# Kernel optimization log

Hardware: AMD Instinct MI355X
Metric: run time of the kernel (lower is better)

The kernel has to match this reference:

```python
import jax, jax.numpy as jnp
import numpy as np

B = 32
SEQ_LEN = 512      # T and n_fft
PRED_LEN = 96      # STFT window_size = PRED_LEN // 2 = 48
TOP_K = 3
D_MODEL = 512
D_FF = 512
N_HEADS = 8
C_OUT = 32         # graph node count
NODE_DIM = 10
CONV_CH = 32
SKIP_CH = 32
GCN_DEPTH = 2
PROP_ALPHA = 0.05
HOP = 48
EPS = 1e-5


def layer_norm(x, g, b):
    m = x.mean(-1, keepdims=True)
    v = ((x - m) ** 2).mean(-1, keepdims=True)
    return (x - m) * jax.lax.rsqrt(v + EPS) * g + b


def stft_mag(x):
    """torch.stft(center=True, hann window of len 48 center-padded to n_fft) magnitude,
    vmapped over channels. Returns [B, frames, n_fft//2+1, N]."""
    n_fft = SEQ_LEN
    win_len = PRED_LEN // 2
    n = jnp.arange(win_len, dtype=x.dtype)
    win = 0.5 - 0.5 * jnp.cos(2.0 * jnp.pi * n / win_len)   # periodic hann
    pad_l = (n_fft - win_len) // 2
    win = jnp.pad(win, (pad_l, n_fft - win_len - pad_l))     # center-pad window to n_fft
    T = x.shape[1]
    xp = jnp.pad(x, ((0, 0), (n_fft // 2, n_fft // 2), (0, 0)), mode='reflect')
    nfr = T // HOP + 1
    idx = jnp.arange(nfr)[:, None] * HOP + jnp.arange(n_fft)[None, :]
    frames = xp[:, idx, :]                                   # [B, nfr, n_fft, N]
    spec = jnp.fft.rfft(frames * win[None, None, :, None], axis=2)
    return jnp.abs(spec)


def attention_block(x, wq, bq, wk, bk, wv, bv, wo, bo, ff1_w, ff1_b, ff2_w, ff2_b,
                    n1_g, n1_b, n2_g, n2_b):
    M, S, D = x.shape
    H, Dh = N_HEADS, D // N_HEADS
    q = (x @ wq.T + bq).reshape(M, S, H, Dh)
    k = (x @ wk.T + bk).reshape(M, S, H, Dh)
    v = (x @ wv.T + bv).reshape(M, S, H, Dh)
    scores = jnp.einsum('mshd,mthd->mhst', q, k) * (1.0 / float(np.sqrt(Dh)))
    o = jnp.einsum('mhst,mthd->mshd', jax.nn.softmax(scores, axis=-1), v).reshape(M, S, D)
    x1 = layer_norm(x + (o @ wo.T + bo), n1_g, n1_b)
    y = jax.nn.gelu(x1 @ ff1_w.T + ff1_b, approximate=False) @ ff2_w.T + ff2_b
    return layer_norm(x1 + y, n2_g, n2_b)


def graph_block(x, nv1, nv2, sw, sb, mw, mb, ew, eb, lw, lb, g, b):
    # adaptive adjacency over C_OUT nodes
    adp = jax.nn.softmax(jax.nn.relu(nv1 @ nv2), axis=1)
    adj = adp + jnp.eye(C_OUT, dtype=x.dtype)
    a = adj / adj.sum(1, keepdims=True)
    # start_conv: [B,1,D,T] -> [B,CONV_CH,C_OUT,T]
    h = jax.lax.conv_general_dilated(x.transpose(0, 2, 1)[:, None], sw, (1, 1), 'VALID',
                                     dimension_numbers=('NCHW', 'OIHW', 'NCHW'))
    h = h + sb[None, :, None, None]
    x0, outs = h, [h]
    for _ in range(GCN_DEPTH):  # mixprop
        h = PROP_ALPHA * x0 + (1.0 - PROP_ALPHA) * jnp.einsum('bcwt,vw->bcvt', h, a)
        outs.append(h)
    ho = jnp.einsum('oc,bcnt->bont', mw, jnp.concatenate(outs, axis=1)) + mb[None, :, None, None]
    h = jax.nn.gelu(ho, approximate=False)
    out = jnp.einsum('bcns,tcs->btn', h, ew) + eb[None, :, None]   # end_conv (1,seq_len) kernel
    out = out @ lw + lb                                            # Linear c_out -> d_model
    return layer_norm(x + out, g, b)


def setup_inputs() -> dict:
    ks = jax.random.split(jax.random.key(0), 32)
    r = lambda i, shape, s=0.02: jax.random.normal(ks[i], shape, jnp.float32) * s
    kh = D_MODEL - C_OUT + 1
    return {
        'x': jax.random.normal(ks[0], (B, SEQ_LEN, D_MODEL), jnp.float32),
        'nv1': r(1, (TOP_K, C_OUT, NODE_DIM), 1.0),
        'nv2': r(2, (TOP_K, NODE_DIM, C_OUT), 1.0),
        'start_w': r(3, (TOP_K, CONV_CH, 1, kh, 1)),
        'start_b': r(4, (TOP_K, CONV_CH)),
        'mix_w': r(5, (TOP_K, SKIP_CH, (GCN_DEPTH + 1) * CONV_CH)),
        'mix_b': r(6, (TOP_K, SKIP_CH)),
        'end_w': r(7, (TOP_K, SEQ_LEN, SKIP_CH, SEQ_LEN)),
        'end_b': r(8, (TOP_K, SEQ_LEN)),
        'glin_w': r(9, (TOP_K, C_OUT, D_MODEL)),
        'glin_b': r(10, (TOP_K, D_MODEL)),
        'gnorm_g': 1.0 + r(11, (TOP_K, D_MODEL), 0.1),
        'gnorm_b': r(12, (TOP_K, D_MODEL), 0.1),
        'wq': r(13, (D_MODEL, D_MODEL)), 'bq': r(14, (D_MODEL,)),
        'wk': r(15, (D_MODEL, D_MODEL)), 'bk': r(16, (D_MODEL,)),
        'wv': r(17, (D_MODEL, D_MODEL)), 'bv': r(18, (D_MODEL,)),
        'wo': r(19, (D_MODEL, D_MODEL)), 'bo': r(20, (D_MODEL,)),
        'ff1_w': r(21, (D_FF, D_MODEL)), 'ff1_b': r(22, (D_FF,)),
        'ff2_w': r(23, (D_MODEL, D_FF)), 'ff2_b': r(24, (D_MODEL,)),
        'an1_g': 1.0 + r(25, (D_MODEL,), 0.1), 'an1_b': r(26, (D_MODEL,), 0.1),
        'an2_g': 1.0 + r(27, (D_MODEL,), 0.1), 'an2_b': r(28, (D_MODEL,), 0.1),
        'norm_g': 1.0 + r(29, (D_MODEL,), 0.1), 'norm_b': r(30, (D_MODEL,), 0.1),
    }


def reference(x, nv1, nv2, start_w, start_b, mix_w, mix_b, end_w, end_b, glin_w, glin_b,
              gnorm_g, gnorm_b, wq, bq, wk, bk, wv, bv, wo, bo,
              ff1_w, ff1_b, ff2_w, ff2_b, an1_g, an1_b, an2_g, an2_b, norm_g, norm_b):
    Bx, T, N = x.shape
    mag = stft_mag(x)                                   # [B, frames, Fbins, N]
    freq = mag.mean(axis=(0, 1, 3)).at[0].set(0.0)
    top = np.asarray(jax.lax.top_k(freq, TOP_K)[1])     # concrete: shapes below are data-dependent
    periods = [int(T // int(f)) for f in top]
    sw = jax.nn.softmax(mag[:, :, top, :].mean(axis=(1, 3)), axis=1)  # [B, k] scale weights
    cur = x
    res = []
    for i in range(TOP_K):
        scale = periods[i]
        # NOTE: faithful to the original bug: x is overwritten by gconv output each iteration
        cur = graph_block(cur, nv1[i], nv2[i], start_w[i], start_b[i], mix_w[i], mix_b[i],
                          end_w[i], end_b[i], glin_w[i], glin_b[i], gnorm_g[i], gnorm_b[i])
        length = -(-T // scale) * scale
        out = jnp.pad(cur, ((0, 0), (0, length - T), (0, 0))) if length > T else cur
        out = out.reshape(Bx * (length // scale), scale, N)
        out = attention_block(out, wq, bq, wk, bk, wv, bv, wo, bo,
                              ff1_w, ff1_b, ff2_w, ff2_b, an1_g, an1_b, an2_g, an2_b)
        out = jax.nn.gelu(layer_norm(out, norm_g, norm_b), approximate=False)
        out = out.reshape(Bx, length, N)[:, :T]
        res.append(out)
    res = jnp.stack(res, axis=-1)                       # [B, T, N, k]
    return (res * sw[:, None, None, :]).sum(-1) + cur
```

## Files before the change

### kernel.cpp

```cpp
#include <hip/hip_runtime.h>
#include <math.h>

#define DI __device__ __forceinline__

namespace {
constexpr int B_ = 32;
constexpr int T_ = 512;
constexpr int N_ = 512;
constexpr int C_ = 32;
constexpr int KH_ = 481;
constexpr int HOP_ = 48;
constexpr int WIN_ = 48;
constexpr int NFR_ = 11;
constexpr int NBIN_ = 257;
constexpr int NSB_ = 8 * NFR_ * B_;
constexpr int TOKMAX = 21760;
constexpr int PLW = TOKMAX * 512;
constexpr float EPS_ = 1e-5f;

constexpr size_t MBY = 1ull << 20;
constexpr size_t OFF_META = 0;
constexpr size_t OFF_FREQ = 4096;
constexpr size_t OFF_SW   = 8192;
constexpr size_t OFF_BEFF = 16384;
constexpr size_t OFF_P12  = 32768;
constexpr size_t OFF_FSB  = 65536;
constexpr size_t OFF_OSM  = 1 * MBY;
constexpr size_t OFF_WB   = 4 * MBY;
constexpr size_t OFF_WDH  = 10 * MBY;
constexpr size_t OFF_EWH  = 12 * MBY;
constexpr size_t OFF_CUR  = 44 * MBY;
constexpr size_t OFF_ACC  = 76 * MBY;
constexpr size_t TR       = 108 * MBY;
constexpr size_t OFF_T    = TR;
constexpr size_t OFF_WPH  = TR + 6 * MBY;
constexpr size_t OFF_G    = TR + 64 * MBY;
constexpr size_t OFF_G2   = TR + 128 * MBY;
constexpr size_t OFF_PART = TR + 192 * MBY;
constexpr size_t OFF_A0 = TR;
constexpr size_t OFF_A2 = TR + 44 * MBY;
constexpr size_t OFF_A3 = TR + 88 * MBY;
constexpr size_t OFF_A4 = TR + 132 * MBY;
constexpr size_t OFF_A5 = TR + 176 * MBY;
constexpr size_t OFF_FP = TR;
}

typedef __attribute__((ext_vector_type(2))) float f32x2;
typedef __attribute__((ext_vector_type(4))) float f32x4;
typedef __attribute__((ext_vector_type(8))) short bf8;
typedef __attribute__((ext_vector_type(8))) unsigned short u16x8;

DI float gelu_exact(float x) { return 0.5f * x * (1.0f + erff(x * 0.7071067811865475f)); }
DI unsigned short f2bf(float f) {
  unsigned u = __float_as_uint(f);
  u += 0x7FFFu + ((u >> 16) & 1u);
  return (unsigned short)(u >> 16);
}
DI float bf2f(unsigned short s) { return __uint_as_float(((unsigned)s) << 16); }
DI float ld2(const unsigned short* __restrict__ H, const unsigned short* __restrict__ L,
             size_t i) { return bf2f(H[i]) + bf2f(L[i]); }
DI void st2(unsigned short* __restrict__ H, unsigned short* __restrict__ L,
            size_t i, float v) {
  unsigned short h = f2bf(v);
  H[i] = h;
  L[i] = f2bf(v - bf2f(h));
}
DI void gll16(const unsigned short* g, unsigned short* l) {
  __builtin_amdgcn_global_load_lds(
      (const __attribute__((address_space(1))) void*)g,
      (__attribute__((address_space(3))) void*)l, 16, 0, 0);
}

__global__ __launch_bounds__(256) void k_stft2(const float* __restrict__ x,
                                               float* __restrict__ fpart) {
  int bid = blockIdx.x;
  int cc = bid & 7;
  int f = (bid >> 3) % NFR_;
  int b = bid / (8 * NFR_);
  __shared__ float xw[WIN_][64];
  int tid = threadIdx.x;
  for (int i = tid; i < WIN_ * 64; i += 256) {
    int j = i >> 6, n = i & 63;
    int gi = f * HOP_ + 232 + j - 256;
    if (gi < 0) gi = -gi;
    float w = 0.5f - 0.5f * cosf((float)j * 0.13089969389957472f);
    xw[j][n] = w * x[((size_t)b * T_ + gi) * N_ + cc * 64 + n];
  }
  __syncthreads();
  for (int pair = tid; pair < NBIN_ * 8; pair += 256) {
    int k = pair >> 3;
    int c4 = (pair & 7) * 4;
    int r0 = (k * 232) & 511;
    float a0 = (float)r0 * 0.012271846303085130f;
    float c = cosf(a0), s = sinf(a0);
    float dA = (float)k * 0.012271846303085130f;
    float cd = cosf(dA), sd = sinf(dA);
    f32x2 ri[8];
#pragma unroll
    for (int q = 0; q < 8; ++q) ri[q] = (f32x2){0.f, 0.f};
#pragma unroll 4
    for (int j = 0; j < WIN_; ++j) {
      float4 v0 = *(const float4*)&xw[j][c4];
      float4 v1 = *(const float4*)&xw[j][32 + c4];
      f32x2 cs = (f32x2){c, s};
      ri[0] += v0.x * cs;
      ri[1] += v0.y * cs;
      ri[2] += v0.z * cs;
      ri[3] += v0.w * cs;
      ri[4] += v1.x * cs;
      ri[5] += v1.y * cs;
      ri[6] += v1.z * cs;
      ri[7] += v1.w * cs;
      float cn = c * cd - s * sd;
      s = s * cd + c * sd;
      c = cn;
    }
    float m = 0.f;
#pragma unroll
    for (int q = 0; q < 8; ++q) m += sqrtf(ri[q].x * ri[q].x + ri[q].y * ri[q].y);
    for (int off = 4; off > 0; off >>= 1) m += __shfl_xor(m, off);
    if ((tid & 7) == 0) fpart[(size_t)k * NSB_ + bid] = m;
  }
}

__global__ __launch_bounds__(256) void k_fred(const float* __restrict__ fpart,
                                              float* __restrict__ freq,
                                              float* __restrict__ fsumb) {
  int k = blockIdx.x;
  int tid = threadIdx.x;
  int b = tid >> 3, j = tid & 7;
  float s = 0.f;
  for (int i = j; i < 88; i += 8) s += fpart[(size_t)k * NSB_ + b * 88 + i];
  for (int off = 4; off > 0; off >>= 1) s += __shfl_xor(s, off);
  __shared__ float bs[32];
  if (j == 0) bs[b] = s;
  __syncthreads();
  if (tid < 32) {
    float v = bs[tid];
    fsumb[k * 32 + tid] = v;
    for (int off = 16; off > 0; off >>= 1) v += __shfl_xor(v, off);
    if (tid == 0) freq[k] = v;
  }
}

__global__ void k_topk(const float* __restrict__ freq, const float* __restrict__ fsumb,
                       int* __restrict__ meta, float* __restrict__ swb) {
  __shared__ int stop[3];
  int tid = threadIdx.x;
  if (tid == 0) {
    float bv[3] = {-1e30f, -1e30f, -1e30f};
    int bi[3] = {1, 1, 1};
    for (int k = 1; k < NBIN_; ++k) {
      float v = freq[k];
      if (v > bv[0]) { bv[2]=bv[1]; bi[2]=bi[1]; bv[1]=bv[0]; bi[1]=bi[0]; bv[0]=v; bi[0]=k; }
      else if (v > bv[1]) { bv[2]=bv[1]; bi[2]=bi[1]; bv[1]=v; bi[1]=k; }
      else if (v > bv[2]) { bv[2]=v; bi[2]=k; }
    }
    for (int i = 0; i < 3; ++i) {
      int top = bi[i];
      int p = T_ / top;
      int L = ((T_ + p - 1) / p) * p;
      meta[i] = top;
      meta[3 + i] = p;
      meta[6 + i] = L;
      meta[9 + i] = L / p;
      meta[15 + i] = B_ * L;
      stop[i] = top;
    }
  }
  __syncthreads();
  int b = tid;
  if (b < B_) {
    float inv = 1.0f / (float)(NFR_ * N_);
    float m0 = fsumb[stop[0] * 32 + b] * inv;
    float m1 = fsumb[stop[1] * 32 + b] * inv;
    float m2 = fsumb[stop[2] * 32 + b] * inv;
    float mx = fmaxf(m0, fmaxf(m1, m2));
    float e0 = expf(m0 - mx), e1 = expf(m1 - mx), e2 = expf(m2 - mx);
    float s = e0 + e1 + e2;
    swb[b * 4 + 0] = e0 / s; swb[b * 4 + 1] = e1 / s; swb[b * 4 + 2] = e2 / s;
  }
}

__global__ __launch_bounds__(1024) void k_adjprep(const float* __restrict__ nv1,
                                                  const float* __restrict__ nv2,
                                                  const float* __restrict__ mw,
                                                  const float* __restrict__ mb,
                                                  const float* __restrict__ sb,
                                                  float* __restrict__ P12,
                                                  float* __restrict__ beff) {
  __shared__ float A32s[32][32];
  __shared__ float Ms[32][32], P1s[32][32], P2s[32][32], S1[32], S2[32], sbl[32];
  int tid = threadIdx.x;
  if (tid < 32) {
    int v = tid;
    float row[32];
    for (int w = 0; w < 32; ++w) {
      float s = 0.f;
      for (int d = 0; d < 10; ++d) s += nv1[v * 10 + d] * nv2[d * 32 + w];
      row[w] = fmaxf(s, 0.f);
    }
    float mx = -1e30f;
    for (int w = 0; w < 32; ++w) mx = fmaxf(mx, row[w]);
    float sm = 0.f;
    for (int w = 0; w < 32; ++w) { row[w] = expf(row[w] - mx); sm += row[w]; }
    for (int w = 0; w < 32; ++w) row[w] /= sm;
    row[v] += 1.0f;
    float rs = 0.f;
    for (int w = 0; w < 32; ++w) rs += row[w];
    for (int w = 0; w < 32; ++w) A32s[v][w] = row[w] / rs;
    sbl[tid] = sb[tid];
  }
  __syncthreads();
  int w = tid >> 5, v = tid & 31;
  Ms[w][v] = A32s[v][w];
  __syncthreads();
  float p1 = 0.95f * Ms[w][v] + (w == v ? 0.05f : 0.f);
  P1s[w][v] = p1;
  __syncthreads();
  float p2 = 0.f;
  for (int u = 0; u < 32; ++u) p2 += P1s[w][u] * Ms[u][v];
  p2 = 0.95f * p2 + (w == v ? 0.05f : 0.f);
  P2s[w][v] = p2;
  P12[tid] = p1;
  P12[1024 + tid] = p2;
  __syncthreads();
  if (tid < 32) {
    float s1 = 0.f, s2 = 0.f;
    for (int u = 0; u < 32; ++u) { s1 += P1s[u][tid]; s2 += P2s[u][tid]; }
    S1[tid] = s1; S2[tid] = s2;
  }
  __syncthreads();
  int o = w;
  float be = mb[o];
  for (int c = 0; c < 32; ++c) {
    float sc = sbl[c];
    be += mw[o * 96 + c] * sc;
    be += mw[o * 96 + 32 + c] * sc * S1[v];
    be += mw[o * 96 + 64 + c] * sc * S2[v];
  }
  beff[tid] = be;
}

__global__ __launch_bounds__(256) void k_T(const float* __restrict__ P12,
                                           const float* __restrict__ mw,
                                           float* __restrict__ Tm) {
  int idx = blockIdx.x * 256 + threadIdx.x;
  int r = idx >> 10, k2 = idx & 1023;
  int o = r >> 5, v = r & 31;
  int c = k2 >> 5, w = k2 & 31;
  float t = mw[o * 96 + 32 + c] * P12[w * 32 + v]
          + mw[o * 96 + 64 + c] * P12[1024 + w * 32 + v];
  if (w == v) t += mw[o * 96 + c];
  Tm[idx] = t;
}

__global__ void k_wdh(const float* __restrict__ swi, unsigned short* __restrict__ WH) {
  int idx = blockIdx.x * 256 + threadIdx.x;
  int j = idx >> 10, k2 = idx & 1023;
  int c = k2 >> 5, w = k2 & 31;
  int kk = j - w;
  float vv = (kk >= 0 && kk < KH_) ? swi[c * KH_ + kk] : 0.f;
  WH[idx] = f2bf(vv);
}

__global__ void k_splith(const float* __restrict__ src, unsigned short* __restrict__ Hi,
                         int n) {
  int i = blockIdx.x * 256 + threadIdx.x;
  if (i * 4 >= n) return;
  float4 v = *(const float4*)&src[i * 4];
  ushort4 h;
  h.x = f2bf(v.x); h.y = f2bf(v.y); h.z = f2bf(v.z); h.w = f2bf(v.w);
  *(ushort4*)&Hi[i * 4] = h;
}

__global__ __launch_bounds__(256, 2) void k_mm2(
    const float* __restrict__ A, const unsigned short* __restrict__ Bh,
    const float* __restrict__ bias,
    float* __restrict__ C, float* __restrict__ Cpart,
    int M, int N, int K, int lda, int dogelu) {
  const int bm = blockIdx.y * 128;
  if (bm >= M) return;
  const int bn = blockIdx.x * 128;
  const int nz = gridDim.z, z = blockIdx.z;
  const int kpb = K / nz;
  const int kbeg = z * kpb, kend = kbeg + kpb;

  __shared__ __align__(16) unsigned short AhS[4096], AlS[4096], BhS[4096];

  const int tid = threadIdx.x;
  const int wave = tid >> 6, lane = tid & 63;
  const int wr = wave >> 1, wc = wave & 1;
  const int fr = lane & 15, fs = lane >> 4;

  const int sr = tid >> 1, ss = (tid & 1) * 2;
  const int sx = (sr >> 1) & 3;
  const int so0 = sr * 32 + 8 * (ss ^ sx);
  const int so1 = sr * 32 + 8 * ((ss + 1) ^ sx);

  const int row0 = tid >> 2;
  const int s0 = (tid & 3) ^ ((row0 >> 1) & 3);
  const unsigned short* gBh0 = Bh + (size_t)(bn + row0) * K + s0 * 8;
  const unsigned short* gBh1 = gBh0 + (size_t)64 * K;
  unsigned short* lB0 = &BhS[wave * 512];
  unsigned short* lB1 = &BhS[2048 + wave * 512];

  int aoff[4], boff[4];
#pragma unroll
  for (int m = 0; m < 4; ++m) {
    int ra = wr * 64 + m * 16 + fr;
    aoff[m] = ra * 32 + 8 * (fs ^ ((ra >> 1) & 3));
    int rb = wc * 64 + m * 16 + fr;
    boff[m] = rb * 32 + 8 * (fs ^ ((rb >> 1) & 3));
  }

  const bool aok = (bm + sr) < M;
  const float* Arow = A + (size_t)(bm + sr) * lda + ss * 8;

  f32x4 acc[4][4];
#pragma unroll
  for (int m = 0; m < 4; ++m)
#pragma unroll
    for (int n = 0; n < 4; ++n) acc[m][n] = (f32x4){0.f, 0.f, 0.f, 0.f};

  for (int k0 = kbeg; k0 < kend; k0 += 32) {
    float4 a0, a1, a2, a3;
    if (aok) {
      const float4* p = (const float4*)(Arow + k0);
      a0 = p[0]; a1 = p[1]; a2 = p[2]; a3 = p[3];
    } else {
      a0 = a1 = a2 = a3 = make_float4(0.f, 0.f, 0.f, 0.f);
    }
    float av[16];
    av[0]=a0.x; av[1]=a0.y; av[2]=a0.z; av[3]=a0.w;
    av[4]=a1.x; av[5]=a1.y; av[6]=a1.z; av[7]=a1.w;
    av[8]=a2.x; av[9]=a2.y; av[10]=a2.z; av[11]=a2.w;
    av[12]=a3.x; av[13]=a3.y; av[14]=a3.z; av[15]=a3.w;
    u16x8 h0, h1, l0, l1;
#pragma unroll
    for (int j = 0; j < 8; ++j) {
      unsigned u = __float_as_uint(av[j]);
      h0[j] = (unsigned short)(u >> 16);
      float r2 = av[j] - __uint_as_float(u & 0xffff0000u);
      l0[j] = (unsigned short)(__float_as_uint(r2) >> 16);
      unsigned u2 = __float_as_uint(av[j + 8]);
      h1[j] = (unsigned short)(u2 >> 16);
      float r3 = av[j + 8] - __uint_as_float(u2 & 0xffff0000u);
      l1[j] = (unsigned short)(__float_as_uint(r3) >> 16);
    }
    __syncthreads();
    gll16(gBh0 + k0, lB0); gll16(gBh1 + k0, lB1);
    *(u16x8*)&AhS[so0] = h0; *(u16x8*)&AhS[so1] = h1;
    *(u16x8*)&AlS[so0] = l0; *(u16x8*)&AlS[so1] = l1;
    __syncthreads();
    bf8 ah[4], al4[4], bh4[4];
#pragma unroll
    for (int m = 0; m < 4; ++m) {
      ah[m]  = *(const bf8*)&AhS[aoff[m]];
      al4[m] = *(const bf8*)&AlS[aoff[m]];
    }
#pragma unroll
    for (int n = 0; n < 4; ++n) bh4[n] = *(const bf8*)&BhS[boff[n]];
#pragma unroll
    for (int m = 0; m < 4; ++m)
#pragma unroll
      for (int n = 0; n < 4; ++n) {
        acc[m][n] = __builtin_amdgcn_mfma_f32_16x16x32_bf16(ah[m],  bh4[n], acc[m][n], 0, 0, 0);
        acc[m][n] = __builtin_amdgcn_mfma_f32_16x16x32_bf16(al4[m], bh4[n], acc[m][n], 0, 0, 0);
      }
  }

  if (nz > 1) {
    float* P = Cpart + (size_t)z * M * N;
#pragma unroll
    for (int m = 0; m < 4; ++m)
#pragma unroll
      for (int r = 0; r < 4; ++r) {
        int row = bm + wr * 64 + m * 16 + fs * 4 + r;
        if (row < M) {
#pragma unroll
          for (int n = 0; n < 4; ++n) {
            int col = bn + wc * 64 + n * 16 + fr;
            P[(size_t)row * N + col] = acc[m][n][r];
          }
        }
      }
  } else {
    float bcol[4];
#pragma unroll
    for (int n = 0; n < 4; ++n) bcol[n] = bias ? bias[bn + wc * 64 + n * 16 + fr] : 0.f;
#pragma unroll
    for (int m = 0; m < 4; ++m)
#pragma unroll
      for (int r = 0; r < 4; ++r) {
        int row = bm + wr * 64 + m * 16 + fs * 4 + r;
        if (row < M) {
#pragma unroll
          for (int n = 0; n < 4; ++n) {
            int col = bn + wc * 64 + n * 16 + fr;
            float v = acc[m][n][r] + bcol[n];
            if (dogelu) v = gelu_exact(v);
            C[(size_t)row * N + col] = v;
          }
        }
      }
  }
}

__global__ __launch_bounds__(256, 4) void k_mmb1(
    const unsigned short* __restrict__ Ah,
    const unsigned short* __restrict__ Bh,
    const float* __restrict__ bias,
    unsigned short* __restrict__ Ch, unsigned short* __restrict__ Cl,
    int M, int N, int K, const int* __restrict__ Mdyn, int dogelu) {
  if (Mdyn) M = *Mdyn;
  const int bm = blockIdx.y * 128;
  if (bm >= M) return;
  const int bn = blockIdx.x * 128;

  __shared__ __align__(16) unsigned short AhS[4096], BhS[4096];

  const int tid = threadIdx.x;
  const int wave = tid >> 6, lane = tid & 63;
  const int wr = wave >> 1, wc = wave & 1;
  const int fr = lane & 15, fs = lane >> 4;

  const int row0 = tid >> 2;
  const int s0 = (tid & 3) ^ ((row0 >> 1) & 3);
  const unsigned short* gAh0 = Ah + (size_t)(bm + row0) * K + s0 * 8;
  const unsigned short* gAh1 = gAh0 + (size_t)64 * K;
  const unsigned short* gBh0 = Bh + (size_t)(bn + row0) * K + s0 * 8;
  const unsigned short* gBh1 = gBh0 + (size_t)64 * K;
  const int lb0 = wave * 512, lb1 = 2048 + wave * 512;

  int aoff[4], boff[4];
#pragma unroll
  for (int m = 0; m < 4; ++m) {
    int ra = wr * 64 + m * 16 + fr;
    aoff[m] = ra * 32 + 8 * (fs ^ ((ra >> 1) & 3));
    int rb = wc * 64 + m * 16 + fr;
    boff[m] = rb * 32 + 8 * (fs ^ ((rb >> 1) & 3));
  }

  f32x4 acc[4][4];
#pragma unroll
  for (int m = 0; m < 4; ++m)
#pragma unroll
    for (int n = 0; n < 4; ++n) acc[m][n] = (f32x4){0.f, 0.f, 0.f, 0.f};

  for (int k0 = 0; k0 < K; k0 += 32) {
    __syncthreads();
    gll16(gAh0 + k0, &AhS[lb0]); gll16(gAh1 + k0, &AhS[lb1]);
    gll16(gBh0 + k0, &BhS[lb0]); gll16(gBh1 + k0, &BhS[lb1]);
    __syncthreads();
    bf8 ah[4], bh4[4];
#pragma unroll
    for (int m = 0; m < 4; ++m) ah[m] = *(const bf8*)&AhS[aoff[m]];
#pragma unroll
    for (int n = 0; n < 4; ++n) bh4[n] = *(const bf8*)&BhS[boff[n]];
#pragma unroll
    for (int m = 0; m < 4; ++m)
#pragma unroll
      for (int n = 0; n < 4; ++n)
        acc[m][n] = __builtin_amdgcn_mfma_f32_16x16x32_bf16(ah[m], bh4[n], acc[m][n], 0, 0, 0);
  }

  float bcol[4];
#pragma unroll
  for (int n = 0; n < 4; ++n) bcol[n] = bias[bn + wc * 64 + n * 16 + fr];
#pragma unroll
  for (int m = 0; m < 4; ++m)
#pragma unroll
    for (int r = 0; r < 4; ++r) {
      int row = bm + wr * 64 + m * 16 + fs * 4 + r;
      if (row < M) {
#pragma unroll
        for (int n = 0; n < 4; ++n) {
          int col = bn + wc * 64 + n * 16 + fr;
          float v = acc[m][n][r] + bcol[n];
          if (dogelu) v = gelu_exact(v);
          size_t o = (size_t)row * N + col;
          unsigned short h = f2bf(v);
          Ch[o] = h;
          if (Cl) Cl[o] = f2bf(v - bf2f(h));
        }
      }
    }
}

__global__ __launch_bounds__(256, 4) void k_mmqkv(
    const unsigned short* __restrict__ Ah,
    const unsigned short* __restrict__ Bh,
    const float* __restrict__ bq, const float* __restrict__ bk,
    const float* __restrict__ bv,
    unsigned short* __restrict__ Qh, unsigned short* __restrict__ Kh,
    unsigned short* __restrict__ Vh,
    int M, int K, const int* __restrict__ Mdyn) {
  if (Mdyn) M = *Mdyn;
  const int bm = blockIdx.y * 128;
  if (bm >= M) return;
  const int bn = blockIdx.x * 128;
  const int sel = bn >> 9;
  unsigned short* Ch = sel == 0 ? Qh : (sel == 1 ? Kh : Vh);
  const float* bias = sel == 0 ? bq : (sel == 1 ? bk : bv);
  const int cb = bn & 511;

  __shared__ __align__(16) unsigned short AhS[4096], BhS[4096];

  const int tid = threadIdx.x;
  const int wave = tid >> 6, lane = tid & 63;
  const int wr = wave >> 1, wc = wave & 1;
  const int fr = lane & 15, fs = lane >> 4;

  const int row0 = tid >> 2;
  const int s0 = (tid & 3) ^ ((row0 >> 1) & 3);
  const unsigned short* gAh0 = Ah + (size_t)(bm + row0) * K + s0 * 8;
  const unsigned short* gAh1 = gAh0 + (size_t)64 * K;
  const unsigned short* gBh0 = Bh + (size_t)(bn + row0) * K + s0 * 8;
  const unsigned short* gBh1 = gBh0 + (size_t)64 * K;
  const int lb0 = wave * 512, lb1 = 2048 + wave * 512;

  int aoff[4], boff[4];
#pragma unroll
  for (int m = 0; m < 4; ++m) {
    int ra = wr * 64 + m * 16 + fr;
    aoff[m] = ra * 32 + 8 * (fs ^ ((ra >> 1) & 3));
    int rb = wc * 64 + m * 16 + fr;
    boff[m] = rb * 32 + 8 * (fs ^ ((rb >> 1) & 3));
  }

  f32x4 acc[4][4];
#pragma unroll
  for (int m = 0; m < 4; ++m)
#pragma unroll
    for (int n = 0; n < 4; ++n) acc[m][n] = (f32x4){0.f, 0.f, 0.f, 0.f};

  for (int k0 = 0; k0 < K; k0 += 32) {
    __syncthreads();
    gll16(gAh0 + k0, &AhS[lb0]); gll16(gAh1 + k0, &AhS[lb1]);
    gll16(gBh0 + k0, &BhS[lb0]); gll16(gBh1 + k0, &BhS[lb1]);
    __syncthreads();
    bf8 ah[4], bh4[4];
#pragma unroll
    for (int m = 0; m < 4; ++m) ah[m] = *(const bf8*)&AhS[aoff[m]];
#pragma unroll
    for (int n = 0; n < 4; ++n) bh4[n] = *(const bf8*)&BhS[boff[n]];
#pragma unroll
    for (int m = 0; m < 4; ++m)
#pragma unroll
      for (int n = 0; n < 4; ++n)
        acc[m][n] = __builtin_amdgcn_mfma_f32_16x16x32_bf16(ah[m], bh4[n], acc[m][n], 0, 0, 0);
  }

  float bcol[4];
#pragma unroll
  for (int n = 0; n < 4; ++n) bcol[n] = bias[cb + wc * 64 + n * 16 + fr];
#pragma unroll
  for (int m = 0; m < 4; ++m)
#pragma unroll
    for (int r = 0; r < 4; ++r) {
      int row = bm + wr * 64 + m * 16 + fs * 4 + r;
      if (row < M) {
#pragma unroll
        for (int n = 0; n < 4; ++n) {
          int col = cb + wc * 64 + n * 16 + fr;
          Ch[(size_t)row * 512 + col] = f2bf(acc[m][n][r] + bcol[n]);
        }
      }
    }
}

__global__ void k_red16(const float* __restrict__ part, const float* __restrict__ eb,
                        float* __restrict__ dst) {
  int idx = blockIdx.x * 256 + threadIdx.x;
  float s = eb ? eb[idx & 511] : 0.f;
#pragma unroll
  for (int zz = 0; zz < 16; ++zz) s += part[(size_t)zz * 524288 + idx];
  dst[idx] = s;
}

__global__ void k_redsplit(const float* __restrict__ part, unsigned short* __restrict__ WH) {
  int idx = blockIdx.x * 256 + threadIdx.x;
  float s = 0.f;
#pragma unroll
  for (int zz = 0; zz < 8; ++zz) s += part[(size_t)zz * 524288 + idx];
  WH[idx] = f2bf(s);
}

__global__ __launch_bounds__(256) void k_repack(const float* __restrict__ G,
                                                float* __restrict__ G2) {
  int bid = blockIdx.x;
  int st = bid & 15, c = (bid >> 4) & 31, b = bid >> 9;
  __shared__ float tile[32][33];
  int tid = threadIdx.x;
  int n = tid & 31, s = tid >> 5;
  for (int q = 0; q < 4; ++q) {
    int ss = s + q * 8;
    tile[ss][n] = G[((size_t)b * T_ + st * 32 + ss) * 1024 + c * 32 + n];
  }
  __syncthreads();
  int s2 = tid & 31, n2 = tid >> 5;
  for (int q = 0; q < 4; ++q) {
    int nn = n2 + q * 8;
    G2[((size_t)b * 32 + nn) * 16384 + c * 512 + st * 32 + s2] = tile[s2][nn];
  }
}

__global__ __launch_bounds__(256) void k_lwln(const float* __restrict__ osm,
                                              const float* __restrict__ lw,
                                              const float* __restrict__ lb,
                                              const float* __restrict__ curIn,
                                              const float* __restrict__ g,
                                              const float* __restrict__ bt,
                                              float* __restrict__ curOut,
                                              unsigned short* __restrict__ xh,
                                              unsigned short* __restrict__ xl,
                                              const int* __restrict__ meta, int iter) {
  int tok = blockIdx.x;
  int b = tok >> 9, t = tok & 511;
  __shared__ float os[C_];
  __shared__ float red[256];
  int tid = threadIdx.x;
  if (tid < C_) os[tid] = osm[((size_t)b * C_ + tid) * T_ + t];
  __syncthreads();
  float val[2];
#pragma unroll
  for (int q = 0; q < 2; ++q) {
    int m = tid + q * 256;
    float s = lb[m] + curIn[(size_t)tok * N_ + m];
    for (int n2 = 0; n2 < C_; ++n2) s += os[n2] * lw[n2 * N_ + m];
    val[q] = s;
  }
  red[tid] = val[0] + val[1];
  __syncthreads();
  for (int off = 128; off > 0; off >>= 1) { if (tid < off) red[tid] += red[tid + off]; __syncthreads(); }
  float mean = red[0] * (1.0f / N_);
  __syncthreads();
  float d0 = val[0] - mean, d1 = val[1] - mean;
  red[tid] = d0 * d0 + d1 * d1;
  __syncthreads();
  for (int off = 128; off > 0; off >>= 1) { if (tid < off) red[tid] += red[tid + off]; __syncthreads(); }
  float inv = rsqrtf(red[0] * (1.0f / N_) + EPS_);
  float o0 = d0 * inv * g[tid] + bt[tid];
  float o1 = d1 * inv * g[tid + 256] + bt[tid + 256];
  curOut[(size_t)tok * N_ + tid] = o0;
  curOut[(size_t)tok * N_ + tid + 256] = o1;
  int L = meta[6 + iter];
  size_t pi = ((size_t)b * L + t) * N_;
  st2(xh, xl, pi + tid, o0);
  st2(xh, xl, pi + tid + 256, o1);
}

__global__ void k_padtail(unsigned short* __restrict__ xh, unsigned short* __restrict__ xl,
                          const int* __restrict__ meta, int iter) {
  int L = meta[6 + iter];
  int pad = L - T_;
  if (pad <= 0) return;
  size_t total = (size_t)B_ * pad * N_;
  for (size_t idx = (size_t)blockIdx.x * 256 + threadIdx.x; idx < total;
       idx += (size_t)gridDim.x * 256) {
    size_t row = idx >> 9;
    int d = (int)(idx & 511);
    int b = (int)(row / pad), l = T_ + (int)(row % pad);
    size_t o = ((size_t)b * L + l) * N_ + d;
    xh[o] = 0; xl[o] = 0;
  }
}

__global__ __launch_bounds__(256) void k_lnadd(const unsigned short* __restrict__ r1h,
                                               const unsigned short* __restrict__ r1l,
                                               const unsigned short* __restrict__ r2h,
                                               const unsigned short* __restrict__ r2l,
                                               const float* __restrict__ g,
                                               const float* __restrict__ bt,
                                               unsigned short* __restrict__ dh,
                                               unsigned short* __restrict__ dl,
                                               const int* __restrict__ meta, int iter) {
  int tokens = meta[15 + iter];
  int tok = blockIdx.x;
  if (tok >= tokens) return;
  __shared__ float red[256];
  int tid = threadIdx.x;
  float val[2];
#pragma unroll
  for (int q = 0; q < 2; ++q) {
    size_t i = (size_t)tok * N_ + tid + q * 256;
    val[q] = ld2(r1h, r1l, i) + ld2(r2h, r2l, i);
  }
  red[tid] = val[0] + val[1];
  __syncthreads();
  for (int off = 128; off > 0; off >>= 1) { if (tid < off) red[tid] += red[tid + off]; __syncthreads(); }
  float mean = red[0] * (1.0f / N_);
  __syncthreads();
  float d0 = val[0] - mean, d1 = val[1] - mean;
  red[tid] = d0 * d0 + d1 * d1;
  __syncthreads();
  for (int off = 128; off > 0; off >>= 1) { if (tid < off) red[tid] += red[tid + off]; __syncthreads(); }
  float inv = rsqrtf(red[0] * (1.0f / N_) + EPS_);
  st2(dh, dl, (size_t)tok * N_ + tid, d0 * inv * g[tid] + bt[tid]);
  st2(dh, dl, (size_t)tok * N_ + tid + 256, d1 * inv * g[tid + 256] + bt[tid + 256]);
}

__global__ __launch_bounds__(256) void k_lnfin(const unsigned short* __restrict__ r1h,
                                               const unsigned short* __restrict__ r1l,
                                               const unsigned short* __restrict__ r2h,
                                               const unsigned short* __restrict__ r2l,
                                               const float* __restrict__ g1,
                                               const float* __restrict__ b1,
                                               const float* __restrict__ g2,
                                               const float* __restrict__ b2,
                                               const float* __restrict__ swb,
                                               float* __restrict__ acc,
                                               const int* __restrict__ meta, int iter) {
  int L = meta[6 + iter];
  int tok = blockIdx.x;
  if (tok >= B_ * L) return;
  int b = tok / L, l = tok % L;
  if (l >= T_) return;
  __shared__ float red[256];
  int tid = threadIdx.x;
  float val[2];
#pragma unroll
  for (int q = 0; q < 2; ++q) {
    size_t i = (size_t)tok * N_ + tid + q * 256;
    val[q] = ld2(r1h, r1l, i) + ld2(r2h, r2l, i);
  }
  red[tid] = val[0] + val[1];
  __syncthreads();
  for (int off = 128; off > 0; off >>= 1) { if (tid < off) red[tid] += red[tid + off]; __syncthreads(); }
  float mean = red[0] * (1.0f / N_);
  __syncthreads();
  float d0 = val[0] - mean, d1 = val[1] - mean;
  red[tid] = d0 * d0 + d1 * d1;
  __syncthreads();
  for (int off = 128; off > 0; off >>= 1) { if (tid < off) red[tid] += red[tid + off]; __syncthreads(); }
  float inv = rsqrtf(red[0] * (1.0f / N_) + EPS_);
  float y0 = d0 * inv * g1[tid] + b1[tid];
  float y1 = d1 * inv * g1[tid + 256] + b1[tid + 256];
  __syncthreads();
  red[tid] = y0 + y1;
  __syncthreads();
  for (int off = 128; off > 0; off >>= 1) { if (tid < off) red[tid] += red[tid + off]; __syncthreads(); }
  float mean2 = red[0] * (1.0f / N_);
  __syncthreads();
  float e0 = y0 - mean2, e1 = y1 - mean2;
  red[tid] = e0 * e0 + e1 * e1;
  __syncthreads();
  for (int off = 128; off > 0; off >>= 1) { if (tid < off) red[tid] += red[tid + off]; __syncthreads(); }
  float inv2 = rsqrtf(red[0] * (1.0f / N_) + EPS_);
  float s = swb[b * 4 + iter];
  float u0 = gelu_exact(e0 * inv2 * g2[tid] + b2[tid]);
  float u1 = gelu_exact(e1 * inv2 * g2[tid + 256] + b2[tid + 256]);
  size_t o = ((size_t)b * T_ + l) * N_;
  acc[o + tid] += s * u0;
  acc[o + tid + 256] += s * u1;
}

__global__ __launch_bounds__(256) void k_attn32(
    const unsigned short* __restrict__ qh,
    const unsigned short* __restrict__ kh,
    const unsigned short* __restrict__ vh,
    unsigned short* __restrict__ oh,
    const int* __restrict__ meta, int iter) {
  int S = meta[3 + iter];
  if (S > 32) return;
  int L = meta[6 + iter], nseq = meta[9 + iter];
  int npair = B_ * nseq * 8;
  __shared__ float Kt[4][64 * 33];
  __shared__ unsigned short Vsh[4][32 * 66];
  __shared__ float qs[4][64];
  int tid = threadIdx.x;
  int wave = tid >> 6, lane = tid & 63;
  float* Ktw = Kt[wave];
  unsigned short* Vw = Vsh[wave];
  int gw = (blockIdx.x * 256 + tid) >> 6;
  int nw = (gridDim.x * 256) >> 6;
  const int tt = lane & 31;
  const int hf = lane >> 5;
  for (int pair = gw; pair < npair; pair += nw) {
    int h = pair & 7;
    int m = pair >> 3;
    int b = m / nseq, g2 = m - b * nseq;
    size_t base = ((size_t)b * L + (size_t)g2 * S) * N_ + h * 64;
    for (int i = lane; i < S * 64; i += 64) {
      int t = i >> 6, d = i & 63;
      size_t gi = base + (size_t)t * N_ + d;
      Ktw[d * 33 + t] = bf2f(kh[gi]);
      Vw[t * 66 + d] = vh[gi];
    }
    bool tok = tt < S;
    for (int s = 0; s < S; ++s) {
      qs[wave][lane] = bf2f(qh[base + (size_t)s * N_ + lane]);
      float part = 0.f;
      if (tok) {
        const float* kp = &Ktw[hf * 32 * 33 + tt];
        const float* qp = &qs[wave][hf * 32];
#pragma unroll 8
        for (int j = 0; j < 32; ++j) part += qp[j] * kp[j * 33];
      }
      part += __shfl_xor(part, 32);
      float sc = tok ? part * 0.125f : -3.0e38f;
      float mx = sc;
      for (int off = 16; off > 0; off >>= 1) mx = fmaxf(mx, __shfl_xor(mx, off));
      float p = tok ? expf(sc - mx) : 0.f;
      float ssum = p;
      for (int off = 16; off > 0; off >>= 1) ssum += __shfl_xor(ssum, off);
      float ov = 0.f;
      for (int t = 0; t < S; ++t) {
        float pt = __shfl(p, t);
        ov += pt * bf2f(Vw[t * 66 + lane]);
      }
      oh[base + (size_t)s * N_ + lane] = f2bf(ov / ssum);
    }
  }
}

__global__ __launch_bounds__(512) void k_attn_small(
    const unsigned short* __restrict__ qh,
    const unsigned short* __restrict__ kh,
    const unsigned short* __restrict__ vh,
    unsigned short* __restrict__ oh,
    const int* __restrict__ meta, int iter) {
  int S = meta[3 + iter];
  if (S <= 32 || S > 128) return;
  int L = meta[6 + iter], nseq = meta[9 + iter];
  int M = B_ * nseq;
  int mh = blockIdx.x;
  int m = mh >> 3, h = mh & 7;
  if (m >= M) return;
  int b = m / nseq, g2 = m % nseq;
  size_t tok0 = (size_t)b * L + (size_t)g2 * S;
  __shared__ float Ks[64 * 129];
  __shared__ float Vs[128 * 65];
  __shared__ float qrow[8][64];
  __shared__ float Pr[8][128];
  int tid = threadIdx.x;
  for (int i = tid; i < S * 64; i += 512) {
    int t = i >> 6, d = i & 63;
    size_t gi = (tok0 + t) * N_ + h * 64 + d;
    Ks[d * 129 + t] = bf2f(kh[gi]);
    Vs[t * 65 + d] = bf2f(vh[gi]);
  }
  __syncthreads();
  int wave = tid >> 6, lane = tid & 63;
  for (int s = wave; s < S; s += 8) {
    qrow[wave][lane] = bf2f(qh[(tok0 + s) * N_ + h * 64 + lane]);
    float sc0 = -3.0e38f, sc1 = -3.0e38f;
    if (lane < S) {
      float ad = 0.f;
#pragma unroll 16
      for (int j = 0; j < 64; ++j) ad += qrow[wave][j] * Ks[j * 129 + lane];
      sc0 = ad * 0.125f;
    }
    if (S > 64 && lane + 64 < S) {
      float ad = 0.f;
#pragma unroll 16
      for (int j = 0; j < 64; ++j) ad += qrow[wave][j] * Ks[j * 129 + lane + 64];
      sc1 = ad * 0.125f;
    }
    float mx = fmaxf(sc0, sc1);
    for (int off = 32; off > 0; off >>= 1) mx = fmaxf(mx, __shfl_xor(mx, off));
    float e0 = (lane < S) ? expf(sc0 - mx) : 0.f;
    float e1 = (S > 64 && lane + 64 < S) ? expf(sc1 - mx) : 0.f;
    if (lane < S) Pr[wave][lane] = e0;
    if (S > 64 && lane + 64 < S) Pr[wave][lane + 64] = e1;
    float ssum = e0 + e1;
    for (int off = 32; off > 0; off >>= 1) ssum += __shfl_xor(ssum, off);
    float ov = 0.f;
#pragma unroll 8
    for (int t = 0; t < S; ++t) ov += Pr[wave][t] * Vs[t * 65 + lane];
    oh[(tok0 + s) * N_ + h * 64 + lane] = f2bf(ov / ssum);
  }
}

__global__ __launch_bounds__(256) void k_attn_big(
    const unsigned short* __restrict__ qh,
    const unsigned short* __restrict__ kh,
    const unsigned short* __restrict__ vh,
    unsigned short* __restrict__ oh,
    const int* __restrict__ meta, int iter) {
  int p = meta[3 + iter];
  if (p <= 128) return;
  int L = meta[6 + iter], nseq = meta[9 + iter];
  int M = B_ * nseq;
  int mh = blockIdx.x;
  int m = mh >> 3, h = mh & 7;
  if (m >= M) return;
  int S = p;
  int b = m / nseq, g2 = m % nseq;
  size_t tok0 = (size_t)b * L + (size_t)g2 * S;
  __shared__ unsigned short Ks[512 * 66];
  __shared__ unsigned short Vs[512 * 66];
  __shared__ float qrow[4][64];
  __shared__ float Pr[4][512];
  int tid = threadIdx.x;
  for (int i = tid; i < S * 64; i += 256) {
    int t = i >> 6, d = i & 63;
    size_t gi = (tok0 + t) * N_ + h * 64 + d;
    Ks[t * 66 + d] = kh[gi];
    Vs[t * 66 + d] = vh[gi];
  }
  __syncthreads();
  int wave = tid >> 6, lane = tid & 63;
  for (int s = wave; s < S; s += 4) {
    qrow[wave][lane] = bf2f(qh[(tok0 + s) * N_ + h * 64 + lane]);
    const float2* qp = (const float2*)&qrow[wave][0];
    float sc[8];
    float mx = -3.0e38f;
#pragma unroll
    for (int c2 = 0; c2 < 8; ++c2) {
      int t = lane + c2 * 64;
      float sv = -3.0e38f;
      if (t < S) {
        const unsigned int* kp = (const unsigned int*)&Ks[t * 66];
        float ad = 0.f;
#pragma unroll
        for (int j2 = 0; j2 < 32; ++j2) {
          float2 qq = qp[j2];
          unsigned int kw = kp[j2];
          ad += qq.x * bf2f((unsigned short)(kw & 0xffffu));
          ad += qq.y * bf2f((unsigned short)(kw >> 16));
        }
        sv = ad * 0.125f;
      }
      sc[c2] = sv;
      mx = fmaxf(mx, sv);
    }
    for (int off = 32; off > 0; off >>= 1) mx = fmaxf(mx, __shfl_xor(mx, off));
    float ssum = 0.f;
#pragma unroll
    for (int c2 = 0; c2 < 8; ++c2) {
      int t = lane + c2 * 64;
      float e = 0.f;
      if (t < S) { e = expf(sc[c2] - mx); Pr[wave][t] = e; }
      ssum += e;
    }
    for (int off = 32; off > 0; off >>= 1) ssum += __shfl_xor(ssum, off);
    float inv = 1.0f / ssum;
    float ov = 0.f;
#pragma unroll 8
    for (int t = 0; t < S; ++t) ov += Pr[wave][t] * bf2f(Vs[t * 66 + lane]);
    oh[(tok0 + s) * N_ + h * 64 + lane] = f2bf(ov * inv);
  }
}

__global__ void k_final(const float* __restrict__ acc, const float* __restrict__ cur,
                        float* __restrict__ out) {
  size_t idx = (size_t)blockIdx.x * 256 + threadIdx.x;
  out[idx] = acc[idx] + cur[idx];
}

extern "C" void kernel_launch(void* const* d_in, const int* in_sizes, int n_in,
                              void* d_out, int out_size, void* d_ws, size_t ws_size,
                              hipStream_t stream) {
  (void)in_sizes; (void)n_in; (void)out_size; (void)ws_size;
  const float* x       = (const float*)d_in[0];
  const float* nv1     = (const float*)d_in[1];
  const float* nv2     = (const float*)d_in[2];
  const float* start_w = (const float*)d_in[3];
  const float* start_b = (const float*)d_in[4];
  const float* mix_w   = (const float*)d_in[5];
  const float* mix_b   = (const float*)d_in[6];
  const float* end_w   = (const float*)d_in[7];
  const float* end_b   = (const float*)d_in[8];
  const float* glin_w  = (const float*)d_in[9];
  const float* glin_b  = (const float*)d_in[10];
  const float* gnorm_g = (const float*)d_in[11];
  const float* gnorm_b = (const float*)d_in[12];
  const float* wq = (const float*)d_in[13];
  const float* bq = (const float*)d_in[14];
  const float* wk = (const float*)d_in[15];
  const float* bk = (const float*)d_in[16];
  const float* wv = (const float*)d_in[17];
  const float* bv = (const float*)d_in[18];
  const float* wo = (const float*)d_in[19];
  const float* bo = (const float*)d_in[20];
  const float* ff1w = (const float*)d_in[21];
  const float* ff1b = (const float*)d_in[22];
  const float* ff2w = (const float*)d_in[23];
  const float* ff2b = (const float*)d_in[24];
  const float* an1g = (const float*)d_in[25];
  const float* an1b = (const float*)d_in[26];
  const float* an2g = (const float*)d_in[27];
  const float* an2b = (const float*)d_in[28];
  const float* nrmg = (const float*)d_in[29];
  const float* nrmb = (const float*)d_in[30];

  char* ws = (char*)d_ws;
  int*   meta = (int*)(ws + OFF_META);
  float* freq = (float*)(ws + OFF_FREQ);
  float* swb  = (float*)(ws + OFF_SW);
  float* beff = (float*)(ws + OFF_BEFF);
  float* P12  = (float*)(ws + OFF_P12);
  float* fsumb = (float*)(ws + OFF_FSB);
  float* osm  = (float*)(ws + OFF_OSM);
  unsigned short* WB  = (unsigned short*)(ws + OFF_WB);
  unsigned short* WdH = (unsigned short*)(ws + OFF_WDH);
  unsigned short* EWH = (unsigned short*)(ws + OFF_EWH);
  float* cur  = (float*)(ws + OFF_CUR);
  float* accb = (float*)(ws + OFF_ACC);
  float* fpart = (float*)(ws + OFF_FP);
  float* Tm   = (float*)(ws + OFF_T);
  unsigned short* WPH = (unsigned short*)(ws + OFF_WPH);
  float* G    = (float*)(ws + OFF_G);
  float* G2   = (float*)(ws + OFF_G2);
  float* PART = (float*)(ws + OFF_PART);
  unsigned short* A0h = (unsigned short*)(ws + OFF_A0); unsigned short* A0l = A0h + PLW;
  unsigned short* A2h = (unsigned short*)(ws + OFF_A2); unsigned short* A2l = A2h + PLW;
  unsigned short* A3h = (unsigned short*)(ws + OFF_A3); unsigned short* A3l = A3h + PLW;
  unsigned short* A4h = (unsigned short*)(ws + OFF_A4);
  unsigned short* A5h = (unsigned short*)(ws + OFF_A5); unsigned short* A5l = A5h + PLW;

  hipMemsetAsync(accb, 0, (size_t)B_ * T_ * N_ * 4, stream);

  k_stft2<<<NSB_, 256, 0, stream>>>(x, fpart);
  k_fred<<<NBIN_, 256, 0, stream>>>(fpart, freq, fsumb);
  k_topk<<<1, 64, 0, stream>>>(freq, fsumb, meta, swb);

  const float* wlist[6] = {wq, wk, wv, wo, ff1w, ff2w};
  for (int w = 0; w < 6; ++w)
    k_splith<<<256, 256, 0, stream>>>(wlist[w], WB + (size_t)w * 262144, 262144);
  unsigned short* WqkvH = WB;
  unsigned short* WoH = WB + 3 * 262144;
  unsigned short* F1H = WB + 4 * 262144;
  unsigned short* F2H = WB + 5 * 262144;

  const float* curIn = x;
  for (int i = 0; i < 3; ++i) {
    k_adjprep<<<1, 1024, 0, stream>>>(nv1 + i * C_ * 10, nv2 + i * 10 * C_,
                                      mix_w + i * C_ * 96, mix_b + i * C_,
                                      start_b + i * C_, P12, beff);
    k_T<<<4096, 256, 0, stream>>>(P12, mix_w + i * C_ * 96, Tm);
    k_wdh<<<2048, 256, 0, stream>>>(start_w + i * C_ * KH_, WdH);
    k_mm2<<<dim3(4, 8, 8), 256, 0, stream>>>(Tm, WdH, nullptr, nullptr, PART,
                                             1024, 512, 1024, 1024, 0);
    k_redsplit<<<2048, 256, 0, stream>>>(PART, WPH);
    k_mm2<<<dim3(8, 128, 1), 256, 0, stream>>>(curIn, WPH, beff, G, nullptr,
                                               16384, 1024, 512, 512, 1);
    k_repack<<<B_ * C_ * 16, 256, 0, stream>>>(G, G2);
    k_splith<<<8192, 256, 0, stream>>>(end_w + (size_t)i * 8388608, EWH, 8388608);
    k_mm2<<<dim3(4, 8, 16), 256, 0, stream>>>(G2, EWH, nullptr, nullptr, PART,
                                              1024, 512, 16384, 16384, 0);
    k_red16<<<2048, 256, 0, stream>>>(PART, end_b + i * T_, osm);
    k_lwln<<<B_ * T_, 256, 0, stream>>>(osm, glin_w + i * C_ * N_, glin_b + i * N_, curIn,
                                        gnorm_g + i * N_, gnorm_b + i * N_, cur,
                                        A0h, A0l, meta, i);
    k_padtail<<<512, 256, 0, stream>>>(A0h, A0l, meta, i);
    const int* Mdyn = meta + 15 + i;
    dim3 gT(4, TOKMAX / 128, 1);
    k_mmqkv<<<dim3(12, TOKMAX / 128), 256, 0, stream>>>(A0h, WqkvH, bq, bk, bv,
                                                        A2h, A3h, A4h, TOKMAX, 512, Mdyn);
    k_attn32<<<2048, 256, 0, stream>>>(A2h, A3h, A4h, A5h, meta, i);
    k_attn_small<<<4096, 512, 0, stream>>>(A2h, A3h, A4h, A5h, meta, i);
    k_attn_big<<<1024, 256, 0, stream>>>(A2h, A3h, A4h, A5h, meta, i);
    k_mmb1<<<gT, 256, 0, stream>>>(A5h, WoH, bo, A2h, A2l, TOKMAX, 512, 512, Mdyn, 0);
    k_lnadd<<<TOKMAX, 256, 0, stream>>>(A0h, A0l, A2h, A2l, an1g, an1b, A3h, A3l, meta, i);
    k_mmb1<<<gT, 256, 0, stream>>>(A3h, F1H, ff1b, A4h, nullptr, TOKMAX, 512, 512, Mdyn, 1);
    k_mmb1<<<gT, 256, 0, stream>>>(A4h, F2H, ff2b, A5h, A5l, TOKMAX, 512, 512, Mdyn, 0);
    k_lnfin<<<TOKMAX, 256, 0, stream>>>(A3h, A3l, A5h, A5l, an2g, an2b, nrmg, nrmb,
                                        swb, accb, meta, i);
    curIn = cur;
  }
  k_final<<<(B_ * T_ * N_) / 256, 256, 0, stream>>>(accb, curIn, (float*)d_out);
}
```

Measured before the change: 2.168 ms.

## Store graph conv intermediate as bf16 and use specialized bf16 GEMMs

The graph-block conv GEMM now writes its GELU output directly as bf16 instead of fp32, the repack transposes bf16 tiles, and the end-conv split-K GEMM reads bf16 A through direct global-to-LDS loads instead of converting fp32 on the fly. This halves the memory traffic of the large intermediate G/G2 buffers and removes per-tile fp32-to-bf16 conversion in the K=16384 GEMM. The cost is rounding G to bf16 before the end convolution, which drops any hi/lo split precision the old path may have kept.

```diff
diff --git a/kernel.cpp b/kernel.cpp
--- a/kernel.cpp
+++ b/kernel.cpp
@@ -407,6 +407,160 @@
   }
 }
 
+__global__ __launch_bounds__(256, 4) void k_mmcv(
+    const float* __restrict__ A, const unsigned short* __restrict__ Bh,
+    const float* __restrict__ bias,
+    unsigned short* __restrict__ C,
+    int M, int N, int K, int lda) {
+  const int bm = blockIdx.y * 128;
+  const int bn = blockIdx.x * 128;
+
+  __shared__ __align__(16) unsigned short AhS[4096], BhS[4096];
+
+  const int tid = threadIdx.x;
+  const int wave = tid >> 6, lane = tid & 63;
+  const int wr = wave >> 1, wc = wave & 1;
+  const int fr = lane & 15, fs = lane >> 4;
+
+  const int sr = tid >> 1, ss = (tid & 1) * 2;
+  const int sx = (sr >> 1) & 3;
+  const int so0 = sr * 32 + 8 * (ss ^ sx);
+  const int so1 = sr * 32 + 8 * ((ss + 1) ^ sx);
+
+  const int row0 = tid >> 2;
+  const int s0 = (tid & 3) ^ ((row0 >> 1) & 3);
+  const unsigned short* gBh0 = Bh + (size_t)(bn + row0) * K + s0 * 8;
+  const unsigned short* gBh1 = gBh0 + (size_t)64 * K;
+  unsigned short* lB0 = &BhS[wave * 512];
+  unsigned short* lB1 = &BhS[2048 + wave * 512];
+
+  int aoff[4], boff[4];
+#pragma unroll
+  for (int m = 0; m < 4; ++m) {
+    int ra = wr * 64 + m * 16 + fr;
+    aoff[m] = ra * 32 + 8 * (fs ^ ((ra >> 1) & 3));
+    int rb = wc * 64 + m * 16 + fr;
+    boff[m] = rb * 32 + 8 * (fs ^ ((rb >> 1) & 3));
+  }
+
+  const float* Arow = A + (size_t)(bm + sr) * lda + ss * 8;
+
+  f32x4 acc[4][4];
+#pragma unroll
+  for (int m = 0; m < 4; ++m)
+#pragma unroll
+    for (int n = 0; n < 4; ++n) acc[m][n] = (f32x4){0.f, 0.f, 0.f, 0.f};
+
+  for (int k0 = 0; k0 < K; k0 += 32) {
+    const float4* p = (const float4*)(Arow + k0);
+    float4 a0 = p[0], a1 = p[1], a2 = p[2], a3 = p[3];
+    u16x8 h0, h1;
+    h0[0]=f2bf(a0.x); h0[1]=f2bf(a0.y); h0[2]=f2bf(a0.z); h0[3]=f2bf(a0.w);
+    h0[4]=f2bf(a1.x); h0[5]=f2bf(a1.y); h0[6]=f2bf(a1.z); h0[7]=f2bf(a1.w);
+    h1[0]=f2bf(a2.x); h1[1]=f2bf(a2.y); h1[2]=f2bf(a2.z); h1[3]=f2bf(a2.w);
+    h1[4]=f2bf(a3.x); h1[5]=f2bf(a3.y); h1[6]=f2bf(a3.z); h1[7]=f2bf(a3.w);
+    __syncthreads();
+    gll16(gBh0 + k0, lB0); gll16(gBh1 + k0, lB1);
+    *(u16x8*)&AhS[so0] = h0; *(u16x8*)&AhS[so1] = h1;
+    __syncthreads();
+    bf8 ah[4], bh4[4];
+#pragma unroll
+    for (int m = 0; m < 4; ++m) ah[m] = *(const bf8*)&AhS[aoff[m]];
+#pragma unroll
+    for (int n = 0; n < 4; ++n) bh4[n] = *(const bf8*)&BhS[boff[n]];
+#pragma unroll
+    for (int m = 0; m < 4; ++m)
+#pragma unroll
+      for (int n = 0; n < 4; ++n)
+        acc[m][n] = __builtin_amdgcn_mfma_f32_16x16x32_bf16(ah[m], bh4[n], acc[m][n], 0, 0, 0);
+  }
+
+  float bcol[4];
+#pragma unroll
+  for (int n = 0; n < 4; ++n) bcol[n] = bias[bn + wc * 64 + n * 16 + fr];
+#pragma unroll
+  for (int m = 0; m < 4; ++m)
+#pragma unroll
+    for (int r = 0; r < 4; ++r) {
+      int row = bm + wr * 64 + m * 16 + fs * 4 + r;
+#pragma unroll
+      for (int n = 0; n < 4; ++n) {
+        int col = bn + wc * 64 + n * 16 + fr;
+        C[(size_t)row * N + col] = f2bf(gelu_exact(acc[m][n][r] + bcol[n]));
+      }
+    }
+}
+
+__global__ __launch_bounds__(256, 4) void k_mmend(
+    const unsigned short* __restrict__ Ah, const unsigned short* __restrict__ Bh,
+    float* __restrict__ Cpart, int M, int N, int K) {
+  const int bm = blockIdx.y * 128;
+  const int bn = blockIdx.x * 128;
+  const int nz = gridDim.z, z = blockIdx.z;
+  const int kpb = K / nz;
+  const int kbeg = z * kpb, kend = kbeg + kpb;
+
+  __shared__ __align__(16) unsigned short AhS[4096], BhS[4096];
+
+  const int tid = threadIdx.x;
+  const int wave = tid >> 6, lane = tid & 63;
+  const int wr = wave >> 1, wc = wave & 1;
+  const int fr = lane & 15, fs = lane >> 4;
+
+  const int row0 = tid >> 2;
+  const int s0 = (tid & 3) ^ ((row0 >> 1) & 3);
+  const unsigned short* gAh0 = Ah + (size_t)(bm + row0) * K + s0 * 8;
+  const unsigned short* gAh1 = gAh0 + (size_t)64 * K;
+  const unsigned short* gBh0 = Bh + (size_t)(bn + row0) * K + s0 * 8;
+  const unsigned short* gBh1 = gBh0 + (size_t)64 * K;
+  const int lb0 = wave * 512, lb1 = 2048 + wave * 512;
+
+  int aoff[4], boff[4];
+#pragma unroll
+  for (int m = 0; m < 4; ++m) {
+    int ra = wr * 64 + m * 16 + fr;
+    aoff[m] = ra * 32 + 8 * (fs ^ ((ra >> 1) & 3));
+    int rb = wc * 64 + m * 16 + fr;
+    boff[m] = rb * 32 + 8 * (fs ^ ((rb >> 1) & 3));
+  }
+
+  f32x4 acc[4][4];
+#pragma unroll
+  for (int m = 0; m < 4; ++m)
+#pragma unroll
+    for (int n = 0; n < 4; ++n) acc[m][n] = (f32x4){0.f, 0.f, 0.f, 0.f};
+
+  for (int k0 = kbeg; k0 < kend; k0 += 32) {
+    __syncthreads();
+    gll16(gAh0 + k0, &AhS[lb0]); gll16(gAh1 + k0, &AhS[lb1]);
+    gll16(gBh0 + k0, &BhS[lb0]); gll16(gBh1 + k0, &BhS[lb1]);
+    __syncthreads();
+    bf8 ah[4], bh4[4];
+#pragma unroll
+    for (int m = 0; m < 4; ++m) ah[m] = *(const bf8*)&AhS[aoff[m]];
+#pragma unroll
+    for (int n = 0; n < 4; ++n) bh4[n] = *(const bf8*)&BhS[boff[n]];
+#pragma unroll
+    for (int m = 0; m < 4; ++m)
+#pragma unroll
+      for (int n = 0; n < 4; ++n)
+        acc[m][n] = __builtin_amdgcn_mfma_f32_16x16x32_bf16(ah[m], bh4[n], acc[m][n], 0, 0, 0);
+  }
+
+  float* P = Cpart + (size_t)z * M * N;
+#pragma unroll
+  for (int m = 0; m < 4; ++m)
+#pragma unroll
+    for (int r = 0; r < 4; ++r) {
+      int row = bm + wr * 64 + m * 16 + fs * 4 + r;
+#pragma unroll
+      for (int n = 0; n < 4; ++n) {
+        int col = bn + wc * 64 + n * 16 + fr;
+        P[(size_t)row * N + col] = acc[m][n][r];
+      }
+    }
+}
+
 __global__ __launch_bounds__(256, 4) void k_mmb1(
     const unsigned short* __restrict__ Ah,
     const unsigned short* __restrict__ Bh,
@@ -587,11 +741,11 @@
   WH[idx] = f2bf(s);
 }
 
-__global__ __launch_bounds__(256) void k_repack(const float* __restrict__ G,
-                                                float* __restrict__ G2) {
+__global__ __launch_bounds__(256) void k_repackb(const unsigned short* __restrict__ G,
+                                                 unsigned short* __restrict__ G2) {
   int bid = blockIdx.x;
   int st = bid & 15, c = (bid >> 4) & 31, b = bid >> 9;
-  __shared__ float tile[32][33];
+  __shared__ unsigned short tile[32][34];
   int tid = threadIdx.x;
   int n = tid & 31, s = tid >> 5;
   for (int q = 0; q < 4; ++q) {
@@ -1002,8 +1156,8 @@
   float* fpart = (float*)(ws + OFF_FP);
   float* Tm   = (float*)(ws + OFF_T);
   unsigned short* WPH = (unsigned short*)(ws + OFF_WPH);
-  float* G    = (float*)(ws + OFF_G);
-  float* G2   = (float*)(ws + OFF_G2);
+  unsigned short* Gb  = (unsigned short*)(ws + OFF_G);
+  unsigned short* G2b = (unsigned short*)(ws + OFF_G2);
   float* PART = (float*)(ws + OFF_PART);
   unsigned short* A0h = (unsigned short*)(ws + OFF_A0); unsigned short* A0l = A0h + PLW;
   unsigned short* A2h = (unsigned short*)(ws + OFF_A2); unsigned short* A2l = A2h + PLW;
@@ -1035,12 +1189,10 @@
     k_mm2<<<dim3(4, 8, 8), 256, 0, stream>>>(Tm, WdH, nullptr, nullptr, PART,
                                              1024, 512, 1024, 1024, 0);
     k_redsplit<<<2048, 256, 0, stream>>>(PART, WPH);
-    k_mm2<<<dim3(8, 128, 1), 256, 0, stream>>>(curIn, WPH, beff, G, nullptr,
-                                               16384, 1024, 512, 512, 1);
-    k_repack<<<B_ * C_ * 16, 256, 0, stream>>>(G, G2);
+    k_mmcv<<<dim3(8, 128), 256, 0, stream>>>(curIn, WPH, beff, Gb, 16384, 1024, 512, 512);
+    k_repackb<<<B_ * C_ * 16, 256, 0, stream>>>(Gb, G2b);
     k_splith<<<8192, 256, 0, stream>>>(end_w + (size_t)i * 8388608, EWH, 8388608);
-    k_mm2<<<dim3(4, 8, 16), 256, 0, stream>>>(G2, EWH, nullptr, nullptr, PART,
-                                              1024, 512, 16384, 16384, 0);
+    k_mmend<<<dim3(4, 8, 16), 256, 0, stream>>>(G2b, EWH, PART, 1024, 512, 16384);
     k_red16<<<2048, 256, 0, stream>>>(PART, end_b + i * T_, osm);
     k_lwln<<<B_ * T_, 256, 0, stream>>>(osm, glin_w + i * C_ * N_, glin_b + i * N_, curIn,
                                         gnorm_g + i * N_, gnorm_b + i * N_, cur,
```

Measured after the change: 2.016 ms. 7.0% less time.
